# Performance work log

Hardware: AMD Instinct MI355X
Metric: run time of the kernel (lower is better)

## Reference

```python
import jax, jax.numpy as jnp
import numpy as np

B, S, D, H, HD = 2, 1024, 1024, 16, 64
CKV, CQ, R, DFF, L, V = 256, 384, 32, 2816, 4, 32000
EPS = 1.1920929e-07  # torch RMSNorm default eps = finfo(float32).eps


def rmsnorm(x, w):
    return x * jax.lax.rsqrt(jnp.mean(x * x, -1, keepdims=True) + EPS) * w


def rope(x, base=10000.0):
    # x: [B, H, S, d]; GPT-NeoX style rotate-half, matches RoPE._neg_half
    d, s = x.shape[-1], x.shape[2]
    theta = 1.0 / base ** (jnp.arange(0, d, 2, dtype=jnp.float32) / d)
    ang = jnp.arange(s, dtype=jnp.float32)[:, None] * theta[None, :]
    ang = jnp.concatenate([ang, ang], -1)  # [s, d]
    neg = jnp.concatenate([-x[..., d // 2:], x[..., :d // 2]], -1)
    return x * jnp.cos(ang) + neg * jnp.sin(ang)


def forward(tokens, embed, w_kv_down, b_kv_down, w_q_down, b_q_down, w_kv_up, b_kv_up,
            w_q_up, b_q_up, w_o, b_o, kv_norm_w, q_norm_w, norm1_w, norm2_w,
            w_in, b_in, w_out, b_out, norm_f_w, w_head, b_head):
    h = embed[tokens]                                  # [B, S, D]
    causal = jnp.triu(jnp.ones((S, S), bool), 1)       # True above diagonal -> masked
    scale = np.float32(1.0 / np.sqrt(HD + R))
    for i in range(L):
        xn = rmsnorm(h, norm1_w[i])
        ckv = xn @ w_kv_down[i] + b_kv_down[i]         # [B, S, CKV+R]
        c_kv, k_rope = ckv[..., :CKV], ckv[..., CKV:]
        kv = rmsnorm(c_kv, kv_norm_w[i]) @ w_kv_up[i] + b_kv_up[i]
        kv = kv.reshape(B, S, H, 2 * HD).transpose(0, 2, 1, 3)  # [B, H, S, 2*HD]
        k, v = kv[..., :HD], kv[..., HD:]
        qf = rmsnorm(xn @ w_q_down[i] + b_q_down[i], q_norm_w[i]) @ w_q_up[i] + b_q_up[i]
        qf = qf.reshape(B, S, H, HD + R).transpose(0, 2, 1, 3)   # [B, H, S, HD+R]
        q, q_rope = qf[..., :HD], qf[..., HD:]
        k_rope = rope(k_rope[:, None, :, :])           # [B, 1, S, R], shared across heads
        q_rope = rope(q_rope)
        k = jnp.concatenate([k, jnp.broadcast_to(k_rope, (B, H, S, R))], -1)
        q = jnp.concatenate([q, q_rope], -1)
        a = jnp.einsum('bhqd,bhkd->bhqk', q, k) * scale
        a = jax.nn.softmax(jnp.where(causal, -jnp.inf, a), -1)
        attn = jnp.einsum('bhqk,bhkd->bhqd', a, v).transpose(0, 2, 1, 3).reshape(B, S, D)
        h = h + attn @ w_o[i] + b_o[i]
        uv = rmsnorm(h, norm2_w[i]) @ w_in[i] + b_in[i]  # [B, S, 2*DFF]
        h = h + (uv[..., :DFF] * jax.nn.silu(uv[..., DFF:])) @ w_out[i] + b_out[i]
    return rmsnorm(h, norm_f_w) @ w_head + b_head        # [B, S, V]


def setup_inputs() -> dict:
    key = jax.random.key(0)
    it = iter(jax.random.split(key, 24))
    w = lambda shp: jax.random.normal(next(it), shp, jnp.float32) * 0.02
    return dict(
        tokens=jax.random.randint(next(it), (B, S), 0, V),
        embed=w((V, D)),
        w_kv_down=w((L, D, CKV + R)), b_kv_down=w((L, CKV + R)),
        w_q_down=w((L, D, CQ)), b_q_down=w((L, CQ)),
        w_kv_up=w((L, CKV, 2 * HD * H)), b_kv_up=w((L, 2 * HD * H)),
        w_q_up=w((L, CQ, (HD + R) * H)), b_q_up=w((L, (HD + R) * H)),
        w_o=w((L, D, D)), b_o=w((L, D)),
        kv_norm_w=jnp.ones((L, CKV)), q_norm_w=jnp.ones((L, CQ)),
        norm1_w=jnp.ones((L, D)), norm2_w=jnp.ones((L, D)),
        w_in=w((L, D, 2 * DFF)), b_in=w((L, 2 * DFF)),
        w_out=w((L, DFF, D)), b_out=w((L, D)),
        norm_f_w=jnp.ones((D,)),
        w_head=w((D, V)), b_head=w((V,)),
    )


def reference(tokens, embed, w_kv_down, b_kv_down, w_q_down, b_q_down, w_kv_up, b_kv_up,
              w_q_up, b_q_up, w_o, b_o, kv_norm_w, q_norm_w, norm1_w, norm2_w,
              w_in, b_in, w_out, b_out, norm_f_w, w_head, b_head):
    return forward(tokens, embed, w_kv_down, b_kv_down, w_q_down, b_q_down, w_kv_up,
                   b_kv_up, w_q_up, b_q_up, w_o, b_o, kv_norm_w, q_norm_w, norm1_w,
                   norm2_w, w_in, b_in, w_out, b_out, norm_f_w, w_head, b_head)
```

## Files before the change

### kernel.cpp

```cpp
#include <hip/hip_runtime.h>
#include <cstdint>
#include <cstddef>

typedef unsigned short u16;
typedef __attribute__((__ext_vector_type__(8))) __bf16 bf16x8;
typedef __attribute__((__ext_vector_type__(4))) float f32x4;
typedef __attribute__((__ext_vector_type__(8))) unsigned short u16x8;

#define DEVI __device__ __forceinline__

constexpr int Bb = 2, Ss = 1024, Dd = 1024, Hh = 16;
constexpr int Mm = Bb * Ss;
constexpr int QKD = 128;
constexpr float EPSF = 1.1920929e-07f;
constexpr float NEG = -1e30f;
constexpr float QSCALE = 0.10206207261596577f;
constexpr float LOG1E4_16 = 9.210340371976184f / 16.f;

DEVI u16 f2b(float f) {
  union { float f; uint32_t u; } a; a.f = f;
  uint32_t r = a.u + 0x7FFFu + ((a.u >> 16) & 1u);
  return (u16)(r >> 16);
}
DEVI float b2f(u16 h) {
  union { uint32_t u; float f; } a; a.u = ((uint32_t)h) << 16; return a.f;
}

struct WJob { const float* src; u16* dst; int K; int N; int perm; int ntiles; };
struct WJobs { WJob j[7]; };

__global__ __launch_bounds__(256) void k_wcvt_batch(WJobs jobs, int njobs) {
  int t = blockIdx.x;
  int ji = 0;
  while (ji < njobs - 1 && t >= jobs.j[ji].ntiles) { t -= jobs.j[ji].ntiles; ++ji; }
  const float* __restrict__ src = jobs.j[ji].src;
  u16* __restrict__ dst = jobs.j[ji].dst;
  const int K = jobs.j[ji].K, N = jobs.j[ji].N, perm = jobs.j[ji].perm;
  const int ktiles = K >> 6;
  const int bk = (t % ktiles) * 64;
  const int bn = (t / ktiles) * 64;
  __shared__ float ts[64][65];
  const int tid = threadIdx.x;
  {
    int c4 = tid & 15, r = tid >> 4;
    #pragma unroll
    for (int p = 0; p < 4; ++p) {
      int row = r + p * 16;
      int col = bn + c4 * 4;
      float4 v = make_float4(0.f, 0.f, 0.f, 0.f);
      if (col < N) v = *(const float4*)(src + (size_t)(bk + row) * N + col);
      ts[row][c4 * 4 + 0] = v.x; ts[row][c4 * 4 + 1] = v.y;
      ts[row][c4 * 4 + 2] = v.z; ts[row][c4 * 4 + 3] = v.w;
    }
  }
  __syncthreads();
  {
    int k8 = tid & 7, c = tid >> 3;
    #pragma unroll
    for (int p = 0; p < 2; ++p) {
      int cc = c + p * 32;
      int gcol = bn + cc;
      int row = perm ? ((gcol < 2816) ? (gcol * 2) : ((gcol - 2816) * 2 + 1)) : gcol;
      u16x8 o;
      #pragma unroll
      for (int q = 0; q < 8; ++q) o[q] = f2b(ts[k8 * 8 + q][cc]);
      *(u16x8*)(dst + (size_t)row * K + bk + k8 * 8) = o;
    }
  }
}

__global__ void k_embed(const int* __restrict__ tok, const float* __restrict__ emb,
                        float* __restrict__ h) {
  int m = blockIdx.x;
  int t = tok[m];
  const float4* src = (const float4*)(emb + (size_t)t * Dd);
  float4* dst = (float4*)(h + (size_t)m * Dd);
  dst[threadIdx.x] = src[threadIdx.x];
}

__global__ void k_rms(const float* __restrict__ in, int inStride,
                      const float* __restrict__ w, u16* __restrict__ out, int K) {
  int m = blockIdx.x;
  const float* x = in + (size_t)m * inStride;
  float ss = 0.f;
  for (int i = threadIdx.x; i < K; i += 256) { float v = x[i]; ss += v * v; }
  #pragma unroll
  for (int off = 32; off; off >>= 1) ss += __shfl_xor(ss, off);
  __shared__ float red[4];
  if ((threadIdx.x & 63) == 0) red[threadIdx.x >> 6] = ss;
  __syncthreads();
  float r = rsqrtf((red[0] + red[1] + red[2] + red[3]) / (float)K + EPSF);
  for (int i = threadIdx.x; i < K; i += 256)
    out[(size_t)m * K + i] = f2b(x[i] * r * w[i]);
}

__global__ void k_biascat(const float* __restrict__ b1, const float* __restrict__ b2,
                          float* __restrict__ out) {
  int i = blockIdx.x * 256 + threadIdx.x;
  float v = 0.f;
  if (i < 288) v = b1[i];
  else if (i >= 384) v = b2[i - 384];
  out[i] = v;
}

__global__ void k_buildqk(const float* __restrict__ qf, const float* __restrict__ kv,
                          const float* __restrict__ ckvq, u16* __restrict__ Q,
                          u16* __restrict__ Kb) {
  int s = blockIdx.x, bh = blockIdx.y;
  int b = bh >> 4, h = bh & 15;
  int d = threadIdx.x;
  int m = b * Ss + s;
  int j = d - 64;
  float sn = 0.f, cs = 0.f;
  if (d >= 64 && d < 96) {
    float theta = __expf(-(float)(j & 15) * LOG1E4_16);
    __sincosf((float)s * theta, &sn, &cs);
  }
  const float* qrow = qf + (size_t)m * (Hh * 96) + h * 96;
  float qv = 0.f;
  if (d < 64) qv = qrow[d];
  else if (d < 96) {
    float x = qrow[64 + j], o = qrow[64 + (j ^ 16)];
    qv = x * cs + ((j < 16) ? -o : o) * sn;
  }
  Q[((size_t)bh * Ss + s) * QKD + d] = f2b(qv * QSCALE);
  float kvv = 0.f;
  if (d < 64) kvv = kv[(size_t)m * 2048 + h * 128 + d];
  else if (d < 96) {
    const float* rr = ckvq + (size_t)m * 768 + 256;
    float x = rr[j], o = rr[j ^ 16];
    kvv = x * cs + ((j < 16) ? -o : o) * sn;
  }
  Kb[((size_t)bh * Ss + s) * QKD + d] = f2b(kvv);
}

__global__ void k_buildvt(const float* __restrict__ kv, u16* __restrict__ Vt) {
  __shared__ float t[32][33];
  int bh = blockIdx.x, s0 = blockIdx.y * 32, d0 = blockIdx.z * 32;
  int b = bh >> 4, h = bh & 15;
  int tx = threadIdx.x, ty = threadIdx.y;
  #pragma unroll
  for (int i = ty; i < 32; i += 8) {
    int s = s0 + i, d = d0 + tx;
    t[i][tx] = kv[(size_t)(b * Ss + s) * 2048 + h * 128 + 64 + d];
  }
  __syncthreads();
  #pragma unroll
  for (int i = ty; i < 32; i += 8) {
    int d = d0 + i, s = s0 + tx;
    Vt[((size_t)bh * 64 + d) * Ss + s] = f2b(t[tx][i]);
  }
}

#define GAS __attribute__((address_space(1)))
#define LAS __attribute__((address_space(3)))
DEVI void gll16(const void* g, void* l) {
  __builtin_amdgcn_global_load_lds((GAS const void*)g, (LAS void*)l, 16, 0, 0);
}
#define VMW(n) asm volatile("s_waitcnt vmcnt(" #n ")" ::: "memory")

__global__ __launch_bounds__(256) void k_flash(
    const u16* __restrict__ Qg, const u16* __restrict__ Kg,
    const u16* __restrict__ Vtg, u16* __restrict__ attn) {
  __shared__ u16 lK[64 * 128];
  __shared__ u16 lV[64 * 64];
  __shared__ u16 lP[4][16 * 64];
  const int tid = threadIdx.x;
  const int qt = blockIdx.x, bh = blockIdx.y;
  const int b = bh >> 4, h = bh & 15;
  const int lane = tid & 63, w = tid >> 6;
  const int g = lane >> 4, fr = lane & 15;
  const u16* Qh = Qg + (size_t)bh * Ss * QKD;
  const u16* Kh = Kg + (size_t)bh * Ss * QKD;
  const u16* Vh = Vtg + (size_t)bh * 64 * Ss;

  const int q0 = qt * 64;
  bf16x8 af[4];
  const u16* qrow = Qh + (size_t)(q0 + w * 16 + fr) * QKD + g * 8;
  #pragma unroll
  for (int k4 = 0; k4 < 4; ++k4) af[k4] = *(const bf16x8*)(qrow + k4 * 32);

  f32x4 acc_o[4] = {};
  float mrow = NEG, lrow = 0.f;

  for (int kt = 0; kt <= qt; ++kt) {
    {
      int r = tid >> 4, c = tid & 15;
      #pragma unroll
      for (int gg = 0; gg < 4; ++gg) {
        int row = gg * 16 + r;
        const u16* src = Kh + (size_t)(kt * 64 + row) * QKD + ((c ^ (row & 7)) * 8);
        gll16(src, (u16*)lK + gg * 2048 + tid * 8);
      }
      int r2 = tid >> 3, c2 = tid & 7;
      #pragma unroll
      for (int gg = 0; gg < 2; ++gg) {
        int d = gg * 32 + r2;
        const u16* src = Vh + (size_t)d * Ss + kt * 64 + ((c2 ^ (d & 7)) * 8);
        gll16(src, (u16*)lV + gg * 2048 + tid * 8);
      }
    }
    asm volatile("s_waitcnt vmcnt(0)" ::: "memory");
    __builtin_amdgcn_s_barrier();
    asm volatile("" ::: "memory");

    f32x4 accs[4] = {};
    #pragma unroll
    for (int j = 0; j < 4; ++j) {
      #pragma unroll
      for (int k4 = 0; k4 < 4; ++k4) {
        int row = j * 16 + fr;
        int ch = (k4 * 4 + g) ^ (row & 7);
        bf16x8 kf = *(const bf16x8*)&lK[row * 128 + ch * 8];
        accs[j] = __builtin_amdgcn_mfma_f32_16x16x32_bf16(kf, af[k4], accs[j], 0, 0, 0);
      }
    }

    float p[16];
    float tmax = NEG;
    #pragma unroll
    for (int j = 0; j < 4; ++j)
      #pragma unroll
      for (int r = 0; r < 4; ++r) {
        float s = accs[j][r];
        int kloc = j * 16 + 4 * g + r;
        bool valid = (kt < qt) || (kloc <= w * 16 + fr);
        s = valid ? s : NEG;
        p[j * 4 + r] = s;
        tmax = fmaxf(tmax, s);
      }
    tmax = fmaxf(tmax, __shfl_xor(tmax, 16));
    tmax = fmaxf(tmax, __shfl_xor(tmax, 32));
    float mnew = fmaxf(mrow, tmax);
    float scale = __expf(mrow - mnew);
    float tsum = 0.f;
    #pragma unroll
    for (int i = 0; i < 16; ++i) { p[i] = __expf(p[i] - mnew); tsum += p[i]; }
    tsum += __shfl_xor(tsum, 16);
    tsum += __shfl_xor(tsum, 32);
    lrow = lrow * scale + tsum;
    mrow = mnew;

    #pragma unroll
    for (int j = 0; j < 4; ++j)
      #pragma unroll
      for (int t = 0; t < 2; ++t) {
        uint32_t u = (uint32_t)f2b(p[j * 4 + 2 * t]) |
                     ((uint32_t)f2b(p[j * 4 + 2 * t + 1]) << 16);
        int kp = 8 * j + 2 * g + t;
        int ch = kp >> 2, wi = kp & 3;
        ((uint32_t*)lP[w])[fr * 32 + ((ch ^ (fr & 7)) << 2) + wi] = u;
      }

    float sc_q[4];
    #pragma unroll
    for (int r = 0; r < 4; ++r) sc_q[r] = __shfl(scale, 4 * g + r);
    #pragma unroll
    for (int j2 = 0; j2 < 4; ++j2)
      #pragma unroll
      for (int r = 0; r < 4; ++r) acc_o[j2][r] *= sc_q[r];

    #pragma unroll
    for (int ksub = 0; ksub < 2; ++ksub) {
      int chp = (4 * ksub + g) ^ (fr & 7);
      bf16x8 pa = *(const bf16x8*)&((const u16*)lP[w])[fr * 64 + chp * 8];
      #pragma unroll
      for (int j2 = 0; j2 < 4; ++j2) {
        int d = j2 * 16 + fr;
        int chv = (ksub * 4 + g) ^ (d & 7);
        bf16x8 vf = *(const bf16x8*)&lV[d * 64 + chv * 8];
        acc_o[j2] = __builtin_amdgcn_mfma_f32_16x16x32_bf16(pa, vf, acc_o[j2], 0, 0, 0);
      }
    }
    asm volatile("" ::: "memory");
    __builtin_amdgcn_s_barrier();
    asm volatile("" ::: "memory");
  }

  float li[4];
  #pragma unroll
  for (int r = 0; r < 4; ++r) li[r] = 1.f / __shfl(lrow, 4 * g + r);
  #pragma unroll
  for (int j2 = 0; j2 < 4; ++j2)
    #pragma unroll
    for (int r = 0; r < 4; ++r) {
      int q = q0 + w * 16 + 4 * g + r;
      int d = j2 * 16 + fr;
      attn[((size_t)(b * Ss) + q) * Dd + h * 64 + d] = f2b(acc_o[j2][r] * li[r]);
    }
}

template <int MODE>
__global__ __launch_bounds__(512, 4) void k_gemm256b(
    const u16* __restrict__ A, const u16* __restrict__ Bt,
    const float* __restrict__ bias, void* __restrict__ Cv,
    int N, int K) {
  __shared__ u16 lA[2][128 * 32];
  __shared__ u16 lB[2][256 * 32];
  const int tid = threadIdx.x;
  const int gx = gridDim.x;
  const int nwg = gx * gridDim.y;
  const int f = blockIdx.y * gx + blockIdx.x;
  const int f2 = (f & 7) * (nwg >> 3) + (f >> 3);
  const int bx = f2 % gx, by = f2 / gx;
  const long m0 = (long)bx * 128, n0 = (long)by * 256;
  const int lane = tid & 63, wid = tid >> 6;
  const int wm = (wid >> 2) * 64, wn = (wid & 3) * 64;
  const int fr = lane & 15, l4 = lane >> 4;
  const int sw = (fr >> 1) & 3;

  const int ra = tid >> 2;
  const int ca = ((tid & 3) ^ ((ra >> 1) & 3)) * 8;
  const u16* a0 = A + (m0 + ra) * (long)K + ca;
  const int rb = tid >> 2;
  const int cb0 = ((tid & 3) ^ ((rb >> 1) & 3)) * 8;
  const int cb1 = ((tid & 3) ^ (((rb + 128) >> 1) & 3)) * 8;
  const u16* b0 = Bt + (n0 + rb) * (long)K + cb0;
  const u16* b1 = Bt + (n0 + rb + 128) * (long)K + cb1;

  f32x4 acc[4][4] = {};
  const int NT = K >> 5;

  gll16(a0, (u16*)lA[0] + tid * 8);
  gll16(b0, (u16*)lB[0] + tid * 8);
  gll16(b1, (u16*)lB[0] + 4096 + tid * 8);

  for (int j = 0; j < NT; ++j) {
    const int cur = j & 1;
    const int kk1 = (j + 1) << 5;
    if (j + 1 < NT) {
      gll16(a0 + kk1, (u16*)lA[cur ^ 1] + tid * 8);
      gll16(b0 + kk1, (u16*)lB[cur ^ 1] + tid * 8);
      gll16(b1 + kk1, (u16*)lB[cur ^ 1] + 4096 + tid * 8);
      VMW(3);
    } else {
      VMW(0);
    }
    __builtin_amdgcn_s_barrier();
    asm volatile("" ::: "memory");
    bf16x8 af[4], bfv[4];
    #pragma unroll
    for (int i = 0; i < 4; ++i)
      af[i] = *(const bf16x8*)&lA[cur][(wm + i * 16 + fr) * 32 + ((l4 ^ sw) * 8)];
    #pragma unroll
    for (int jj = 0; jj < 4; ++jj)
      bfv[jj] = *(const bf16x8*)&lB[cur][(wn + jj * 16 + fr) * 32 + ((l4 ^ sw) * 8)];
    #pragma unroll
    for (int i = 0; i < 4; ++i)
      #pragma unroll
      for (int jj = 0; jj < 4; ++jj)
        acc[i][jj] = __builtin_amdgcn_mfma_f32_16x16x32_bf16(af[i], bfv[jj], acc[i][jj], 0, 0, 0);
    asm volatile("" ::: "memory");
    __builtin_amdgcn_s_barrier();
    asm volatile("" ::: "memory");
  }

  const long r0 = m0 + wm + l4 * 4;
  const long c0 = n0 + wn + fr;
  if (MODE == 0) {
    float* C = (float*)Cv;
    #pragma unroll
    for (int j = 0; j < 4; ++j) {
      long col = c0 + j * 16;
      float bs = bias[col];
      #pragma unroll
      for (int i = 0; i < 4; ++i)
        #pragma unroll
        for (int r = 0; r < 4; ++r)
          C[(r0 + i * 16 + r) * (long)N + col] = acc[i][j][r] + bs;
    }
  } else {
    u16* G = (u16*)Cv;
    #pragma unroll
    for (int j = 0; j < 4; ++j) {
      long col = c0 + j * 16;
      int pcol = (int)((col & 1) ? (col >> 1) + 2816 : (col >> 1));
      float bs = bias[pcol];
      #pragma unroll
      for (int i = 0; i < 4; ++i)
        #pragma unroll
        for (int r = 0; r < 4; ++r) {
          float val = acc[i][j][r] + bs;
          float oth = __shfl_xor(val, 1);
          if (!(col & 1)) {
            float x = oth;
            float gv = val * x * (1.f / (1.f + __expf(-x)));
            G[(r0 + i * 16 + r) * 2816L + (col >> 1)] = f2b(gv);
          }
        }
    }
  }
}

template <int MODE, int BN, bool SWZ>
__global__ __launch_bounds__(256) void k_gemm(
    const u16* __restrict__ A, const u16* __restrict__ Bt,
    const float* __restrict__ bias, void* __restrict__ C,
    int N, int K, long sA, long sB, long sC) {
  __shared__ u16 lA[128 * 32];
  __shared__ u16 lB[BN * 32];
  const int tid = threadIdx.x;
  const int bz = blockIdx.z;

  int bx, by;
  if (SWZ) {
    int gx = gridDim.x;
    int nwg = gx * gridDim.y;
    int f = blockIdx.y * gx + blockIdx.x;
    int f2 = (f & 7) * (nwg >> 3) + (f >> 3);
    bx = f2 % gx; by = f2 / gx;
  } else {
    bx = blockIdx.x; by = blockIdx.y;
  }
  const long m0 = (long)bx * 128, n0 = (long)by * BN;

  const u16* Az = A + (size_t)bz * sA;
  const u16* Bz = Bt + (size_t)bz * sB;
  const int srow = tid >> 2;
  const int scol = (tid & 3) << 3;
  const u16* a0 = Az + (m0 + srow) * (long)K + scol;
  const u16* b0 = Bz + (n0 + srow) * (long)K + scol;
  const long rstep = 64L * K;

  const int lane = tid & 63, wid = tid >> 6;
  constexpr int WR = (BN == 128) ? 64 : 32;
  constexpr int MI = WR / 16;
  const int wm = (BN == 128) ? (wid >> 1) * 64 : wid * 32;
  const int wn = (BN == 128) ? (wid & 1) * 64 : 0;
  const int fr = lane & 15, kg = (lane >> 4) * 8;

  f32x4 acc[MI][4] = {};

  for (int kk = 0; kk < K; kk += 32) {
    gll16(a0 + kk, lA + tid * 8);
    gll16(a0 + rstep + kk, lA + 2048 + tid * 8);
    gll16(b0 + kk, lB + tid * 8);
    if (BN == 128) gll16(b0 + rstep + kk, lB + 2048 + tid * 8);
    __syncthreads();
    bf16x8 af[MI], bfr[4];
    #pragma unroll
    for (int i = 0; i < MI; i++) af[i] = *(const bf16x8*)&lA[(wm + i * 16 + fr) * 32 + kg];
    #pragma unroll
    for (int j = 0; j < 4; j++) bfr[j] = *(const bf16x8*)&lB[(wn + j * 16 + fr) * 32 + kg];
    #pragma unroll
    for (int i = 0; i < MI; i++)
      #pragma unroll
      for (int j = 0; j < 4; j++)
        acc[i][j] = __builtin_amdgcn_mfma_f32_16x16x32_bf16(af[i], bfr[j], acc[i][j], 0, 0, 0);
    __syncthreads();
  }

  const int rb = wm + ((lane >> 4) << 2);
  const int cb = wn + (lane & 15);
  #pragma unroll
  for (int j = 0; j < 4; j++) {
    long gcol = n0 + cb + j * 16;
    float bs = 0.f;
    if (gcol < N) bs = bias[gcol];
    #pragma unroll
    for (int i = 0; i < MI; i++) {
      #pragma unroll
      for (int r = 0; r < 4; r++) {
        long grow = m0 + rb + i * 16 + r;
        float val = acc[i][j][r];
        if (MODE == 0) {
          if (gcol < N) ((float*)C)[grow * N + gcol] = val + bs;
        } else {
          if (gcol < N) { float* p = (float*)C + grow * N + gcol; *p += val + bs; }
        }
      }
    }
  }
}

extern "C" void kernel_launch(void* const* d_in, const int* in_sizes, int n_in,
                              void* d_out, int out_size, void* d_ws, size_t ws_size,
                              hipStream_t stream) {
  (void)in_sizes; (void)n_in; (void)out_size; (void)ws_size;
  const int*   tokens    = (const int*)  d_in[0];
  const float* embed     = (const float*)d_in[1];
  const float* w_kv_down = (const float*)d_in[2];
  const float* b_kv_down = (const float*)d_in[3];
  const float* w_q_down  = (const float*)d_in[4];
  const float* b_q_down  = (const float*)d_in[5];
  const float* w_kv_up   = (const float*)d_in[6];
  const float* b_kv_up   = (const float*)d_in[7];
  const float* w_q_up    = (const float*)d_in[8];
  const float* b_q_up    = (const float*)d_in[9];
  const float* w_o       = (const float*)d_in[10];
  const float* b_o       = (const float*)d_in[11];
  const float* kv_norm_w = (const float*)d_in[12];
  const float* q_norm_w  = (const float*)d_in[13];
  const float* norm1_w   = (const float*)d_in[14];
  const float* norm2_w   = (const float*)d_in[15];
  const float* w_in      = (const float*)d_in[16];
  const float* b_in      = (const float*)d_in[17];
  const float* w_out     = (const float*)d_in[18];
  const float* b_out     = (const float*)d_in[19];
  const float* norm_f_w  = (const float*)d_in[20];
  const float* w_head    = (const float*)d_in[21];
  const float* b_head    = (const float*)d_in[22];

  char* base = (char*)d_ws;
  size_t off = 0;
  auto alloc = [&](size_t bytes) -> void* {
    void* p = base + off;
    off += (bytes + 255) & ~(size_t)255;
    return p;
  };
  u16* warena = (u16*)alloc((size_t)32000 * 1024 * 2);
  u16* wT_dq    = warena;
  u16* wT_kvup  = wT_dq   + 768 * 1024;
  u16* wT_qup   = wT_kvup + 2048 * 256;
  u16* wT_o     = wT_qup  + 1536 * 384;
  u16* wT_in    = wT_o    + 1024 * 1024;
  u16* wT_out   = wT_in   + 5632 * 1024;

  float* h     = (float*)alloc((size_t)Mm * 1024 * 4);
  u16*   xn    = (u16*)  alloc((size_t)Mm * 1024 * 2);
  float* ckvq  = (float*)alloc((size_t)Mm * 768 * 4);
  float* bdq   = (float*)alloc(768 * 4);
  u16*   ckvn  = (u16*)  alloc((size_t)Mm * 256 * 2);
  float* kv    = (float*)alloc((size_t)Mm * 2048 * 4);
  u16*   qdn   = (u16*)  alloc((size_t)Mm * 384 * 2);
  float* qf    = (float*)alloc((size_t)Mm * 1536 * 4);
  u16*   Qb    = (u16*)  alloc((size_t)32 * 1024 * QKD * 2);
  u16*   Kb    = (u16*)  alloc((size_t)32 * 1024 * QKD * 2);
  u16*   Vt    = (u16*)  alloc((size_t)32 * 64 * 1024 * 2);
  u16*   attn  = (u16*)  alloc((size_t)Mm * 1024 * 2);
  u16*   gate  = (u16*)  alloc((size_t)Mm * 2816 * 2);

  dim3 tb(32, 8);

  k_embed<<<Mm, 256, 0, stream>>>(tokens, embed, h);

  for (int l = 0; l < 4; l++) {
    WJobs jb;
    jb.j[0] = { w_kv_down + (size_t)l * 1024 * 288,  wT_dq,              1024, 288,  0, 96 };
    jb.j[1] = { w_q_down  + (size_t)l * 1024 * 384,  wT_dq + 384 * 1024, 1024, 384,  0, 96 };
    jb.j[2] = { w_kv_up   + (size_t)l * 256 * 2048,  wT_kvup,            256,  2048, 0, 128 };
    jb.j[3] = { w_q_up    + (size_t)l * 384 * 1536,  wT_qup,             384,  1536, 0, 144 };
    jb.j[4] = { w_o       + (size_t)l * 1024 * 1024, wT_o,               1024, 1024, 0, 256 };
    jb.j[5] = { w_in      + (size_t)l * 1024 * 5632, wT_in,              1024, 5632, 1, 1408 };
    jb.j[6] = { w_out     + (size_t)l * 2816 * 1024, wT_out,             2816, 1024, 0, 704 };
    k_wcvt_batch<<<2832, 256, 0, stream>>>(jb, 7);
    k_biascat<<<3, 256, 0, stream>>>(b_kv_down + l * 288, b_q_down + l * 384, bdq);

    k_rms<<<Mm, 256, 0, stream>>>(h, 1024, norm1_w + l * 1024, xn, 1024);
    k_gemm<0, 64, true><<<dim3(16, 12), 256, 0, stream>>>(xn, wT_dq, bdq,
                                                          ckvq, 768, 1024, 0, 0, 0);
    k_rms<<<Mm, 256, 0, stream>>>(ckvq, 768, kv_norm_w + l * 256, ckvn, 256);
    k_gemm<0, 128, true><<<dim3(16, 16), 256, 0, stream>>>(ckvn, wT_kvup, b_kv_up + l * 2048,
                                                           kv, 2048, 256, 0, 0, 0);
    k_rms<<<Mm, 256, 0, stream>>>(ckvq + 384, 768, q_norm_w + l * 384, qdn, 384);
    k_gemm<0, 128, true><<<dim3(16, 12), 256, 0, stream>>>(qdn, wT_qup, b_q_up + l * 1536,
                                                           qf, 1536, 384, 0, 0, 0);
    k_buildqk<<<dim3(Ss, 32), 128, 0, stream>>>(qf, kv, ckvq, Qb, Kb);
    k_buildvt<<<dim3(32, 32, 2), tb, 0, stream>>>(kv, Vt);
    k_flash<<<dim3(16, 32), 256, 0, stream>>>(Qb, Kb, Vt, attn);
    k_gemm<1, 64, true><<<dim3(16, 16), 256, 0, stream>>>(attn, wT_o, b_o + l * 1024,
                                                          h, 1024, 1024, 0, 0, 0);
    k_rms<<<Mm, 256, 0, stream>>>(h, 1024, norm2_w + l * 1024, xn, 1024);
    k_gemm256b<1><<<dim3(16, 22), 512, 0, stream>>>(xn, wT_in, b_in + l * 5632,
                                                    gate, 5632, 1024);
    k_gemm<1, 64, true><<<dim3(16, 16), 256, 0, stream>>>(gate, wT_out, b_out + l * 1024,
                                                          h, 1024, 2816, 0, 0, 0);
  }

  k_rms<<<Mm, 256, 0, stream>>>(h, 1024, norm_f_w, xn, 1024);
  {
    WJobs jbh;
    jbh.j[0] = { w_head, warena, 1024, 32000, 0, 8000 };
    k_wcvt_batch<<<8000, 256, 0, stream>>>(jbh, 1);
  }
  k_gemm256b<0><<<dim3(16, 125), 512, 0, stream>>>(xn, warena, b_head,
                                                   (float*)d_out, 32000, 1024);
}
```

Baseline: 1.205 ms.

## Double-buffer LDS in flash and GEMM kernels, store kv as bf16

The flash-attention kernel and the generic GEMM now use two LDS buffers and prefetch the next K/V or A/B tile while computing on the current one, with partial vmcnt waits in place of full drains. The kv up-projection GEMM gains a bf16 output mode, so the kv buffer is half the size and the build-QK and build-Vt kernels read bf16 directly. Launch-bound occupancy hints are raised to 6 for both GEMM kernels. This trades doubled LDS use and possible register pressure from the occupancy hint for less load latency stall and less memory traffic. K and V values are now rounded to bf16 before the K RoPE concatenation, which the old path also did, so numerics should be about the same.

```diff
diff --git a/kernel.cpp b/kernel.cpp
--- a/kernel.cpp
+++ b/kernel.cpp
@@ -103,7 +103,7 @@
   out[i] = v;
 }
 
-__global__ void k_buildqk(const float* __restrict__ qf, const float* __restrict__ kv,
+__global__ void k_buildqk(const float* __restrict__ qf, const u16* __restrict__ kv,
                           const float* __restrict__ ckvq, u16* __restrict__ Q,
                           u16* __restrict__ Kb) {
   int s = blockIdx.x, bh = blockIdx.y;
@@ -124,18 +124,18 @@
     qv = x * cs + ((j < 16) ? -o : o) * sn;
   }
   Q[((size_t)bh * Ss + s) * QKD + d] = f2b(qv * QSCALE);
-  float kvv = 0.f;
+  u16 kvv = 0;
   if (d < 64) kvv = kv[(size_t)m * 2048 + h * 128 + d];
   else if (d < 96) {
     const float* rr = ckvq + (size_t)m * 768 + 256;
     float x = rr[j], o = rr[j ^ 16];
-    kvv = x * cs + ((j < 16) ? -o : o) * sn;
-  }
-  Kb[((size_t)bh * Ss + s) * QKD + d] = f2b(kvv);
-}
-
-__global__ void k_buildvt(const float* __restrict__ kv, u16* __restrict__ Vt) {
-  __shared__ float t[32][33];
+    kvv = f2b(x * cs + ((j < 16) ? -o : o) * sn);
+  }
+  Kb[((size_t)bh * Ss + s) * QKD + d] = kvv;
+}
+
+__global__ void k_buildvt(const u16* __restrict__ kv, u16* __restrict__ Vt) {
+  __shared__ u16 t[32][33];
   int bh = blockIdx.x, s0 = blockIdx.y * 32, d0 = blockIdx.z * 32;
   int b = bh >> 4, h = bh & 15;
   int tx = threadIdx.x, ty = threadIdx.y;
@@ -148,7 +148,7 @@
   #pragma unroll
   for (int i = ty; i < 32; i += 8) {
     int d = d0 + i, s = s0 + tx;
-    Vt[((size_t)bh * 64 + d) * Ss + s] = f2b(t[tx][i]);
+    Vt[((size_t)bh * 64 + d) * Ss + s] = t[tx][i];
   }
 }
 
@@ -158,12 +158,13 @@
   __builtin_amdgcn_global_load_lds((GAS const void*)g, (LAS void*)l, 16, 0, 0);
 }
 #define VMW(n) asm volatile("s_waitcnt vmcnt(" #n ")" ::: "memory")
+#define FENCE asm volatile("" ::: "memory")
 
 __global__ __launch_bounds__(256) void k_flash(
     const u16* __restrict__ Qg, const u16* __restrict__ Kg,
     const u16* __restrict__ Vtg, u16* __restrict__ attn) {
-  __shared__ u16 lK[64 * 128];
-  __shared__ u16 lV[64 * 64];
+  __shared__ u16 lK[2][64 * 128];
+  __shared__ u16 lV[2][64 * 64];
   __shared__ u16 lP[4][16 * 64];
   const int tid = threadIdx.x;
   const int qt = blockIdx.x, bh = blockIdx.y;
@@ -174,6 +175,23 @@
   const u16* Kh = Kg + (size_t)bh * Ss * QKD;
   const u16* Vh = Vtg + (size_t)bh * 64 * Ss;
 
+  auto stageKV = [&](int buf, int kt) {
+    int r = tid >> 4, c = tid & 15;
+    #pragma unroll
+    for (int gg = 0; gg < 4; ++gg) {
+      int row = gg * 16 + r;
+      const u16* src = Kh + (size_t)(kt * 64 + row) * QKD + ((c ^ (row & 7)) * 8);
+      gll16(src, (u16*)lK[buf] + gg * 2048 + tid * 8);
+    }
+    int r2 = tid >> 3, c2 = tid & 7;
+    #pragma unroll
+    for (int gg = 0; gg < 2; ++gg) {
+      int d = gg * 32 + r2;
+      const u16* src = Vh + (size_t)d * Ss + kt * 64 + ((c2 ^ (d & 7)) * 8);
+      gll16(src, (u16*)lV[buf] + gg * 2048 + tid * 8);
+    }
+  };
+
   const int q0 = qt * 64;
   bf16x8 af[4];
   const u16* qrow = Qh + (size_t)(q0 + w * 16 + fr) * QKD + g * 8;
@@ -183,26 +201,14 @@
   f32x4 acc_o[4] = {};
   float mrow = NEG, lrow = 0.f;
 
+  stageKV(0, 0);
+
   for (int kt = 0; kt <= qt; ++kt) {
-    {
-      int r = tid >> 4, c = tid & 15;
-      #pragma unroll
-      for (int gg = 0; gg < 4; ++gg) {
-        int row = gg * 16 + r;
-        const u16* src = Kh + (size_t)(kt * 64 + row) * QKD + ((c ^ (row & 7)) * 8);
-        gll16(src, (u16*)lK + gg * 2048 + tid * 8);
-      }
-      int r2 = tid >> 3, c2 = tid & 7;
-      #pragma unroll
-      for (int gg = 0; gg < 2; ++gg) {
-        int d = gg * 32 + r2;
-        const u16* src = Vh + (size_t)d * Ss + kt * 64 + ((c2 ^ (d & 7)) * 8);
-        gll16(src, (u16*)lV + gg * 2048 + tid * 8);
-      }
-    }
-    asm volatile("s_waitcnt vmcnt(0)" ::: "memory");
+    const int cur = kt & 1;
+    if (kt < qt) { stageKV(cur ^ 1, kt + 1); VMW(6); }
+    else { VMW(0); }
     __builtin_amdgcn_s_barrier();
-    asm volatile("" ::: "memory");
+    FENCE;
 
     f32x4 accs[4] = {};
     #pragma unroll
@@ -211,7 +217,7 @@
       for (int k4 = 0; k4 < 4; ++k4) {
         int row = j * 16 + fr;
         int ch = (k4 * 4 + g) ^ (row & 7);
-        bf16x8 kf = *(const bf16x8*)&lK[row * 128 + ch * 8];
+        bf16x8 kf = *(const bf16x8*)&lK[cur][row * 128 + ch * 8];
         accs[j] = __builtin_amdgcn_mfma_f32_16x16x32_bf16(kf, af[k4], accs[j], 0, 0, 0);
       }
     }
@@ -268,13 +274,13 @@
       for (int j2 = 0; j2 < 4; ++j2) {
         int d = j2 * 16 + fr;
         int chv = (ksub * 4 + g) ^ (d & 7);
-        bf16x8 vf = *(const bf16x8*)&lV[d * 64 + chv * 8];
+        bf16x8 vf = *(const bf16x8*)&lV[cur][d * 64 + chv * 8];
         acc_o[j2] = __builtin_amdgcn_mfma_f32_16x16x32_bf16(pa, vf, acc_o[j2], 0, 0, 0);
       }
     }
-    asm volatile("" ::: "memory");
+    FENCE;
     __builtin_amdgcn_s_barrier();
-    asm volatile("" ::: "memory");
+    FENCE;
   }
 
   float li[4];
@@ -291,7 +297,7 @@
 }
 
 template <int MODE>
-__global__ __launch_bounds__(512, 4) void k_gemm256b(
+__global__ __launch_bounds__(512, 6) void k_gemm256b(
     const u16* __restrict__ A, const u16* __restrict__ Bt,
     const float* __restrict__ bias, void* __restrict__ Cv,
     int N, int K) {
@@ -337,7 +343,7 @@
       VMW(0);
     }
     __builtin_amdgcn_s_barrier();
-    asm volatile("" ::: "memory");
+    FENCE;
     bf16x8 af[4], bfv[4];
     #pragma unroll
     for (int i = 0; i < 4; ++i)
@@ -350,9 +356,9 @@
       #pragma unroll
       for (int jj = 0; jj < 4; ++jj)
         acc[i][jj] = __builtin_amdgcn_mfma_f32_16x16x32_bf16(af[i], bfv[jj], acc[i][jj], 0, 0, 0);
-    asm volatile("" ::: "memory");
+    FENCE;
     __builtin_amdgcn_s_barrier();
-    asm volatile("" ::: "memory");
+    FENCE;
   }
 
   const long r0 = m0 + wm + l4 * 4;
@@ -393,12 +399,12 @@
 }
 
 template <int MODE, int BN, bool SWZ>
-__global__ __launch_bounds__(256) void k_gemm(
+__global__ __launch_bounds__(256, 6) void k_gemm(
     const u16* __restrict__ A, const u16* __restrict__ Bt,
     const float* __restrict__ bias, void* __restrict__ C,
     int N, int K, long sA, long sB, long sC) {
-  __shared__ u16 lA[128 * 32];
-  __shared__ u16 lB[BN * 32];
+  __shared__ u16 lA[2][128 * 32];
+  __shared__ u16 lB[2][BN * 32];
   const int tid = threadIdx.x;
   const int bz = blockIdx.z;
 
@@ -430,24 +436,44 @@
   const int fr = lane & 15, kg = (lane >> 4) * 8;
 
   f32x4 acc[MI][4] = {};
-
-  for (int kk = 0; kk < K; kk += 32) {
-    gll16(a0 + kk, lA + tid * 8);
-    gll16(a0 + rstep + kk, lA + 2048 + tid * 8);
-    gll16(b0 + kk, lB + tid * 8);
-    if (BN == 128) gll16(b0 + rstep + kk, lB + 2048 + tid * 8);
-    __syncthreads();
+  const int NT = K >> 5;
+
+  gll16(a0, (u16*)lA[0] + tid * 8);
+  gll16(a0 + rstep, (u16*)lA[0] + 2048 + tid * 8);
+  gll16(b0, (u16*)lB[0] + tid * 8);
+  if (BN == 128) gll16(b0 + rstep, (u16*)lB[0] + 2048 + tid * 8);
+
+  for (int j = 0; j < NT; ++j) {
+    const int cur = j & 1;
+    const int kk1 = (j + 1) << 5;
+    if (j + 1 < NT) {
+      gll16(a0 + kk1, (u16*)lA[cur ^ 1] + tid * 8);
+      gll16(a0 + rstep + kk1, (u16*)lA[cur ^ 1] + 2048 + tid * 8);
+      gll16(b0 + kk1, (u16*)lB[cur ^ 1] + tid * 8);
+      if (BN == 128) {
+        gll16(b0 + rstep + kk1, (u16*)lB[cur ^ 1] + 2048 + tid * 8);
+        VMW(4);
+      } else {
+        VMW(3);
+      }
+    } else {
+      VMW(0);
+    }
+    __builtin_amdgcn_s_barrier();
+    FENCE;
     bf16x8 af[MI], bfr[4];
     #pragma unroll
-    for (int i = 0; i < MI; i++) af[i] = *(const bf16x8*)&lA[(wm + i * 16 + fr) * 32 + kg];
-    #pragma unroll
-    for (int j = 0; j < 4; j++) bfr[j] = *(const bf16x8*)&lB[(wn + j * 16 + fr) * 32 + kg];
+    for (int i = 0; i < MI; i++) af[i] = *(const bf16x8*)&lA[cur][(wm + i * 16 + fr) * 32 + kg];
+    #pragma unroll
+    for (int jj = 0; jj < 4; jj++) bfr[jj] = *(const bf16x8*)&lB[cur][(wn + jj * 16 + fr) * 32 + kg];
     #pragma unroll
     for (int i = 0; i < MI; i++)
       #pragma unroll
-      for (int j = 0; j < 4; j++)
-        acc[i][j] = __builtin_amdgcn_mfma_f32_16x16x32_bf16(af[i], bfr[j], acc[i][j], 0, 0, 0);
-    __syncthreads();
+      for (int jj = 0; jj < 4; jj++)
+        acc[i][jj] = __builtin_amdgcn_mfma_f32_16x16x32_bf16(af[i], bfr[jj], acc[i][jj], 0, 0, 0);
+    FENCE;
+    __builtin_amdgcn_s_barrier();
+    FENCE;
   }
 
   const int rb = wm + ((lane >> 4) << 2);
@@ -463,10 +489,14 @@
       for (int r = 0; r < 4; r++) {
         long grow = m0 + rb + i * 16 + r;
         float val = acc[i][j][r];
-        if (MODE == 0) {
-          if (gcol < N) ((float*)C)[grow * N + gcol] = val + bs;
-        } else {
-          if (gcol < N) { float* p = (float*)C + grow * N + gcol; *p += val + bs; }
+        if (gcol < N) {
+          if (MODE == 0) {
+            ((float*)C)[grow * N + gcol] = val + bs;
+          } else if (MODE == 1) {
+            float* p = (float*)C + grow * N + gcol; *p += val + bs;
+          } else {
+            ((u16*)C)[grow * N + gcol] = f2b(val + bs);
+          }
         }
       }
     }
@@ -521,7 +551,7 @@
   float* ckvq  = (float*)alloc((size_t)Mm * 768 * 4);
   float* bdq   = (float*)alloc(768 * 4);
   u16*   ckvn  = (u16*)  alloc((size_t)Mm * 256 * 2);
-  float* kv    = (float*)alloc((size_t)Mm * 2048 * 4);
+  u16*   kv    = (u16*)  alloc((size_t)Mm * 2048 * 2);
   u16*   qdn   = (u16*)  alloc((size_t)Mm * 384 * 2);
   float* qf    = (float*)alloc((size_t)Mm * 1536 * 4);
   u16*   Qb    = (u16*)  alloc((size_t)32 * 1024 * QKD * 2);
@@ -550,7 +580,7 @@
     k_gemm<0, 64, true><<<dim3(16, 12), 256, 0, stream>>>(xn, wT_dq, bdq,
                                                           ckvq, 768, 1024, 0, 0, 0);
     k_rms<<<Mm, 256, 0, stream>>>(ckvq, 768, kv_norm_w + l * 256, ckvn, 256);
-    k_gemm<0, 128, true><<<dim3(16, 16), 256, 0, stream>>>(ckvn, wT_kvup, b_kv_up + l * 2048,
+    k_gemm<2, 128, true><<<dim3(16, 16), 256, 0, stream>>>(ckvn, wT_kvup, b_kv_up + l * 2048,
                                                            kv, 2048, 256, 0, 0, 0);
     k_rms<<<Mm, 256, 0, stream>>>(ckvq + 384, 768, q_norm_w + l * 384, qdn, 384);
     k_gemm<0, 128, true><<<dim3(16, 12), 256, 0, stream>>>(qdn, wT_qup, b_q_up + l * 1536,
```

New measurement: 2.455 ms. 104% more time.
